# Kernel tuning notes

Measured on AMD Instinct MI355X. Metric: run time of the kernel, lower is better.

The kernel has to match this reference:

```python
import jax, jax.numpy as jnp
import numpy as np

BS, SL, WPL, NP = 32, 256, 4, 320
WD, PD, RD, HD = 768, 64, 64, 256
PN, RN, PL = 32, 64, 8
NF = 128
WINDOW_SIZES = (2, 3, 4)
FD = 2 * HD  # node feature dim


def setup_inputs() -> dict:
    key = jax.random.key(0)
    ks = jax.random.split(key, 24)
    s = 0.02
    inp = {}
    # forward tensors (bert_out stands in for BertModel output after CLS slice)
    inp["bert_out"] = jax.random.normal(ks[0], (BS, NP, WD), jnp.float32)
    inp["wordpiece_gather_idx"] = jax.random.randint(ks[1], (BS, SL, WPL), 0, NP + 1)
    inp["pos"] = jax.random.randint(ks[2], (BS, SL), 0, PN)
    inp["deprel"] = jax.random.randint(ks[3], (BS, SL), 0, RN)
    inp["path"] = jax.random.randint(ks[4], (BS, SL, PL), 0, 2 * SL + 1)
    inp["aspect_head"] = jax.random.randint(ks[5], (BS, SL), 0, SL + 1)
    inp["text_mask"] = jax.random.randint(ks[6], (BS, SL), 0, 2)
    inp["aspect_mask"] = jax.random.randint(ks[7], (BS, SL), 0, 2)
    # parameters (pad row 0 zeroed to mimic padding_idx)
    inp["pos_emb"] = (jax.random.normal(ks[8], (PN, PD)) * s).at[0].set(0.0)
    inp["deprel_emb"] = (jax.random.normal(ks[9], (RN, RD)) * s).at[0].set(0.0)
    inp["pathdepth_emb"] = (jax.random.normal(ks[10], (PL + 2, PD)) * s).at[0].set(0.0)
    inp["ext_rel"] = jax.random.normal(ks[11], (RD,)) * s
    inp["fc1_W"] = jax.random.normal(ks[12], (WD + 2 * PD, FD)) * s
    inp["fc1_b"] = jnp.zeros((FD,), jnp.float32)
    inp["bilin_W"] = jax.random.normal(ks[13], (2 * FD, RD)) * s
    inp["bilin_b"] = jnp.zeros((), jnp.float32)
    inp["W_k2"] = jax.random.normal(ks[14], (2, FD, NF)) * s
    inp["b_k2"] = jnp.zeros((NF,), jnp.float32)
    inp["W_k3"] = jax.random.normal(ks[15], (3, FD, NF)) * s
    inp["b_k3"] = jnp.zeros((NF,), jnp.float32)
    inp["W_k4"] = jax.random.normal(ks[16], (4, FD, NF)) * s
    inp["b_k4"] = jnp.zeros((NF,), jnp.float32)
    inp["fc_out_W"] = jax.random.normal(ks[17], (NF * 3, 3)) * s
    inp["fc_out_b"] = jnp.zeros((3,), jnp.float32)
    return inp


def reference(bert_out, wordpiece_gather_idx, pos, deprel, path, aspect_head,
              text_mask, aspect_mask, pos_emb, deprel_emb, pathdepth_emb, ext_rel,
              fc1_W, fc1_b, bilin_W, bilin_b,
              W_k2, b_k2, W_k3, b_k3, W_k4, b_k4, fc_out_W, fc_out_b):
    bs, sl = pos.shape
    wd = bert_out.shape[-1]
    fd = fc1_b.shape[0]
    # --- wordpiece -> word averaging (pad piece 0 is a zero vector) ---
    pieces = jnp.concatenate([jnp.zeros((bs, 1, wd), bert_out.dtype), bert_out], axis=1)  # [B, NP+1, WD]
    g = jnp.take_along_axis(pieces, wordpiece_gather_idx.reshape(bs, -1)[..., None], axis=1)
    g = g.reshape(bs, sl, -1, wd)                                   # [B, SL, WPL, WD]
    npieces = (wordpiece_gather_idx != 0).sum(-1, keepdims=True)    # [B, SL, 1]
    word = g.sum(2) / jnp.maximum(npieces, 1).astype(g.dtype)       # [B, SL, WD]
    # --- node features ---
    path_depth = (path != 0).sum(-1)                                # [B, SL]
    node_in = jnp.concatenate([word, pos_emb[pos], pathdepth_emb[path_depth]], -1)
    node = jax.nn.relu(node_in @ fc1_W + fc1_b)                     # [B, SL, FD]
    # --- edge features: gather head nodes (0 = pad word -> zeros) ---
    node_pad = jnp.concatenate([jnp.zeros((bs, 1, fd), node.dtype), node], axis=1)
    dep = jnp.take_along_axis(node_pad, aspect_head[..., None], axis=1)  # [B, SL, FD]
    head_text = jnp.concatenate([dep, node], axis=1)                # [B, 2SL, FD]
    tail_text = jnp.concatenate([node, jnp.zeros_like(node)], axis=1)
    edge = jnp.concatenate([head_text, tail_text], axis=-1)         # [B, 2SL, 2FD]
    label = jnp.concatenate([deprel_emb[deprel],
                             jnp.broadcast_to(ext_rel, (bs, sl, ext_rel.shape[0]))], axis=1)
    # bilinear score: x1^T W x2 + b, single output channel
    score = jax.nn.sigmoid(jnp.einsum('bnd,dr,bnr->bn', edge, bilin_W, label) + bilin_b)
    edge_score = jnp.concatenate([jnp.ones((bs, 1), score.dtype), score], axis=1)  # [B, 2SL+1]
    # --- node weight: product of edge scores along dependency path ---
    nw = jnp.prod(jnp.take_along_axis(edge_score[:, None, :], path, axis=2), -1)   # [B, SL]
    nw = jnp.where((text_mask != 0) & (aspect_mask == 0), nw, jnp.zeros_like(nw))
    weight_norm = nw.sum(-1)                                        # [B]
    # --- manual windowed CNN + max pool ---
    pooled = []
    for W, b in ((W_k2, b_k2), (W_k3, b_k3), (W_k4, b_k4)):
        kw = W.shape[0]
        cn = sl - kw + 1
        w_win = jnp.mean(jnp.stack([nw[:, k:k + cn] for k in range(kw)], -1), -1)  # [B, CN]
        y = sum(jnp.einsum('bnf,fm->bnm', node[:, k:k + cn, :], W[k]) for k in range(kw))
        y = w_win[..., None] * y + b                                # [B, CN, NF]
        pooled.append(y.max(axis=1))                                # [B, NF]
    sentence = jnp.concatenate(pooled, -1)
    predicts = sentence @ fc_out_W + fc_out_b                       # [B, 3]
    return predicts, weight_norm
```

## Files before the change

### kernel.cpp

```cpp
#include <hip/hip_runtime.h>
#include <hip/hip_bf16.h>
#include <math.h>

#define BSZ 32
#define SL 256
#define WPL 4
#define NP 320
#define WD 768
#define PD 64
#define RD 64
#define FD 512
#define PL 8
#define NF 128
#define ES_STRIDE 513
#define MROWS (BSZ * SL)
#define NZ 384
#define KZ 2048

typedef __attribute__((ext_vector_type(8))) short bf16x8;
typedef __attribute__((ext_vector_type(4))) float f32x4;
typedef unsigned short ushort_t;
typedef __attribute__((ext_vector_type(4))) ushort_t u16x4;

__device__ __forceinline__ ushort_t f2bf(float x) {
    __hip_bfloat16 h = __float2bfloat16(x);
    return *reinterpret_cast<ushort_t*>(&h);
}
__device__ __forceinline__ float bf2f(ushort_t u) {
    return __uint_as_float(((unsigned)u) << 16);
}

#define NB_GATHER MROWS
#define B_WW   NB_GATHER
#define NB_WW  384
#define B_TAB  (B_WW + NB_WW)
#define NB_TAB 42
#define B_WZT  (B_TAB + NB_TAB)
#define NB_WZT 576
#define B_PAD  (B_WZT + NB_WZT)
#define NB_PAD 2
#define B_UT   (B_PAD + NB_PAD)
#define NB_UT  258
#define NB_TOTAL (B_UT + NB_UT)

__global__ __launch_bounds__(256) void setup_kernel(
    const float* __restrict__ bert, const int* __restrict__ wgi,
    const int* __restrict__ pos, const int* __restrict__ path,
    const float* __restrict__ pos_emb, const float* __restrict__ pd_emb,
    const float* __restrict__ bilin_W, const float* __restrict__ deprel_emb,
    const float* __restrict__ ext_rel, const float* __restrict__ fc1_W,
    const float* __restrict__ fc1_b,
    const float* __restrict__ W2, const float* __restrict__ W3,
    const float* __restrict__ W4,
    ushort_t* __restrict__ word, int* __restrict__ depth,
    ushort_t* __restrict__ Ww, float* __restrict__ posc, float* __restrict__ pdc,
    ushort_t* __restrict__ WzT, ushort_t* __restrict__ node,
    float* __restrict__ Ut, float* __restrict__ v)
{
    const int tid = threadIdx.x;
    const int blk = blockIdx.x;
    if (blk < NB_GATHER) {
        const int bs = blk;
        const int b = bs >> 8;
        const int* gi = wgi + (size_t)bs * WPL;
        const int i0 = gi[0], i1 = gi[1], i2 = gi[2], i3 = gi[3];
        const int npc = (i0 != 0) + (i1 != 0) + (i2 != 0) + (i3 != 0);
        const float inv = 1.0f / (float)(npc > 1 ? npc : 1);
        if (tid < 192) {
            const float4* r0 = (const float4*)(bert + ((size_t)b * NP + (i0 - 1)) * WD);
            const float4* r1 = (const float4*)(bert + ((size_t)b * NP + (i1 - 1)) * WD);
            const float4* r2 = (const float4*)(bert + ((size_t)b * NP + (i2 - 1)) * WD);
            const float4* r3 = (const float4*)(bert + ((size_t)b * NP + (i3 - 1)) * WD);
            float4 s = make_float4(0.f, 0.f, 0.f, 0.f);
            if (i0) { float4 t = r0[tid]; s.x += t.x; s.y += t.y; s.z += t.z; s.w += t.w; }
            if (i1) { float4 t = r1[tid]; s.x += t.x; s.y += t.y; s.z += t.z; s.w += t.w; }
            if (i2) { float4 t = r2[tid]; s.x += t.x; s.y += t.y; s.z += t.z; s.w += t.w; }
            if (i3) { float4 t = r3[tid]; s.x += t.x; s.y += t.y; s.z += t.z; s.w += t.w; }
            u16x4 o;
            o[0] = f2bf(s.x * inv); o[1] = f2bf(s.y * inv);
            o[2] = f2bf(s.z * inv); o[3] = f2bf(s.w * inv);
            *reinterpret_cast<u16x4*>(&word[(size_t)bs * WD + tid * 4]) = o;
        } else if (tid == 192) {
            const int* pp = path + (size_t)bs * PL;
            int pd = 0;
#pragma unroll
            for (int l = 0; l < PL; ++l) pd += (pp[l] != 0);
            depth[bs] = pd;
        }
        return;
    }
    if (blk < B_TAB) {
        __shared__ float s[32][33];
        const int t = blk - B_WW;
        const int kt = t % 24, nt = t / 24;
#pragma unroll
        for (int i = 0; i < 4; ++i) {
            const int idx = i * 256 + tid;
            const int kk = idx >> 5, nn = idx & 31;
            s[kk][nn] = fc1_W[(size_t)(kt * 32 + kk) * FD + nt * 32 + nn];
        }
        __syncthreads();
#pragma unroll
        for (int i = 0; i < 4; ++i) {
            const int idx = i * 256 + tid;
            const int nn = idx >> 5, kk = idx & 31;
            Ww[(size_t)(nt * 32 + nn) * WD + kt * 32 + kk] = f2bf(s[kk][nn]);
        }
        return;
    }
    if (blk < B_WZT) {
        const int r = blk - B_TAB;
#pragma unroll
        for (int h = 0; h < 2; ++h) {
            const int cc = tid + h * 256;
            if (r < 32) {
                float acc = fc1_b[cc];
#pragma unroll
                for (int j = 0; j < PD; ++j)
                    acc += pos_emb[r * PD + j] * fc1_W[(size_t)(WD + j) * FD + cc];
                posc[(size_t)r * FD + cc] = acc;
            } else {
                const int r2 = r - 32;
                float acc = 0.f;
#pragma unroll
                for (int j = 0; j < PD; ++j)
                    acc += pd_emb[r2 * PD + j] * fc1_W[(size_t)(WD + PD + j) * FD + cc];
                pdc[(size_t)r2 * FD + cc] = acc;
            }
        }
        return;
    }
    if (blk < B_PAD) {
        __shared__ float s[32][33];
        const int t2 = blk - B_WZT;
        const int p = t2 / 64, tt = t2 % 64;
        const int dt = tt & 15, ft = tt >> 4;
        int w, k; const float* src;
        if (p < 2)      { w = 0; k = p;     src = W2; }
        else if (p < 5) { w = 1; k = p - 2; src = W3; }
        else            { w = 2; k = p - 5; src = W4; }
#pragma unroll
        for (int i = 0; i < 4; ++i) {
            const int idx = i * 256 + tid;
            const int dd = idx >> 5, ff = idx & 31;
            s[dd][ff] = src[((size_t)k * FD + dt * 32 + dd) * NF + ft * 32 + ff];
        }
        __syncthreads();
#pragma unroll
        for (int i = 0; i < 4; ++i) {
            const int idx = i * 256 + tid;
            const int ff = idx >> 5, dd = idx & 31;
            WzT[(size_t)(w * NF + ft * 32 + ff) * KZ + k * FD + dt * 32 + dd] = f2bf(s[dd][ff]);
        }
        return;
    }
    if (blk < B_UT) {
        const int local = (blk - B_PAD) * 256 + tid;
#pragma unroll
        for (int j = 0; j < 3; ++j) node[(size_t)MROWS * FD + local * 3 + j] = 0;
        return;
    }
    {
        const int idx = (blk - B_UT) * 256 + tid;
        if (idx < 65536) {
            const int r = idx >> 10, d = idx & 1023;
            float s = 0.f;
#pragma unroll
            for (int j = 0; j < RD; ++j) s += bilin_W[d * RD + j] * deprel_emb[r * RD + j];
            Ut[idx] = s;
        } else if (idx < 65536 + FD) {
            const int d = idx - 65536;
            float s = 0.f;
#pragma unroll
            for (int j = 0; j < RD; ++j) s += bilin_W[d * RD + j] * ext_rel[j];
            v[d] = s;
        }
        return;
    }
}

__global__ __launch_bounds__(256) void gemm_node(
    const ushort_t* __restrict__ A,
    const ushort_t* __restrict__ Bt,
    const int* __restrict__ pos, const int* __restrict__ depth,
    const float* __restrict__ posc, const float* __restrict__ pdc,
    ushort_t* __restrict__ C)
{
    __shared__ ushort_t As[128 * 64];
    __shared__ ushort_t Bs[64 * 64];
    __shared__ int spos[128], sdep[128];
    const int tid = threadIdx.x;
    const int wid = tid >> 6, lane = tid & 63;
    const int wr = wid >> 1, wc = wid & 1;
    const int row0 = blockIdx.y * 128, col0 = blockIdx.x * 64;
    const int lr = lane & 15, lk = lane >> 4;
    if (tid < 128) { spos[tid] = pos[row0 + tid]; sdep[tid] = depth[row0 + tid]; }
    f32x4 acc[4][2] = {};
    const ushort_t* gA0 = A + (size_t)row0 * WD;
    const ushort_t* gB0 = Bt + (size_t)col0 * WD;
    for (int k0 = 0; k0 < WD; k0 += 64) {
#pragma unroll
        for (int i = 0; i < 4; ++i) {
            const int c = i * 256 + (wid << 6) + lane;
            const int r = c >> 3, q = (c & 7) ^ (r & 7);
            __builtin_amdgcn_global_load_lds(
                (const __attribute__((address_space(1))) void*)(gA0 + (size_t)r * WD + k0 + q * 8),
                (__attribute__((address_space(3))) void*)((char*)As + i * 4096 + (wid << 10)),
                16, 0, 0);
        }
#pragma unroll
        for (int i = 0; i < 2; ++i) {
            const int c = i * 256 + (wid << 6) + lane;
            const int r = c >> 3, q = (c & 7) ^ (r & 7);
            __builtin_amdgcn_global_load_lds(
                (const __attribute__((address_space(1))) void*)(gB0 + (size_t)r * WD + k0 + q * 8),
                (__attribute__((address_space(3))) void*)((char*)Bs + i * 4096 + (wid << 10)),
                16, 0, 0);
        }
        __syncthreads();
        bf16x8 af[4][2], bfv[2][2];
#pragma unroll
        for (int m = 0; m < 4; ++m) {
            const int fr = wr * 64 + m * 16 + lr;
#pragma unroll
            for (int ks = 0; ks < 2; ++ks)
                af[m][ks] = *reinterpret_cast<const bf16x8*>(
                    &As[fr * 64 + ((((ks << 2) | lk) ^ (fr & 7)) << 3)]);
        }
#pragma unroll
        for (int n = 0; n < 2; ++n) {
            const int fr = wc * 32 + n * 16 + lr;
#pragma unroll
            for (int ks = 0; ks < 2; ++ks)
                bfv[n][ks] = *reinterpret_cast<const bf16x8*>(
                    &Bs[fr * 64 + ((((ks << 2) | lk) ^ (fr & 7)) << 3)]);
        }
#pragma unroll
        for (int ks = 0; ks < 2; ++ks)
#pragma unroll
            for (int m = 0; m < 4; ++m)
#pragma unroll
                for (int n = 0; n < 2; ++n)
                    acc[m][n] = __builtin_amdgcn_mfma_f32_16x16x32_bf16(
                        af[m][ks], bfv[n][ks], acc[m][n], 0, 0, 0);
        __syncthreads();
    }
#pragma unroll
    for (int n = 0; n < 2; ++n) {
        const int col = col0 + wc * 32 + n * 16 + lr;
#pragma unroll
        for (int m = 0; m < 4; ++m) {
            const f32x4 vv = acc[m][n];
#pragma unroll
            for (int j = 0; j < 4; ++j) {
                const int rloc = wr * 64 + m * 16 + lk * 4 + j;
                const float bv = posc[(size_t)spos[rloc] * FD + col]
                               + pdc[(size_t)sdep[rloc] * FD + col];
                C[(size_t)(row0 + rloc) * FD + col] = f2bf(fmaxf(vv[j] + bv, 0.f));
            }
        }
    }
}

__global__ __launch_bounds__(256) void score_kernel(
    const ushort_t* __restrict__ node, const int* __restrict__ aspect_head,
    const int* __restrict__ deprel, const float* __restrict__ Ut,
    const float* __restrict__ v, const float* __restrict__ bilin_b,
    float* __restrict__ edge_score)
{
    const int g = blockIdx.x * 4 + (threadIdx.x >> 6);
    const int lane = threadIdx.x & 63;
    const int b = g >> 9;
    const int n = g & 511;
    const int d0 = lane * 8;
    typedef __attribute__((ext_vector_type(8))) unsigned short u16x8;
    float sum = 0.f;
    if (n < SL) {
        const int dr = deprel[b * SL + n];
        const int h = aspect_head[b * SL + n];
        const float* uc = Ut + (size_t)dr * 1024;
        const u16x8 nv = *reinterpret_cast<const u16x8*>(&node[((size_t)b * SL + n) * FD + d0]);
        if (h != 0) {
            const u16x8 dv = *reinterpret_cast<const u16x8*>(&node[((size_t)b * SL + (h - 1)) * FD + d0]);
#pragma unroll
            for (int i = 0; i < 8; ++i) sum += bf2f(dv[i]) * uc[d0 + i];
        }
#pragma unroll
        for (int i = 0; i < 8; ++i) sum += bf2f(nv[i]) * uc[FD + d0 + i];
    } else {
        const u16x8 nv = *reinterpret_cast<const u16x8*>(&node[((size_t)b * SL + (n - SL)) * FD + d0]);
#pragma unroll
        for (int i = 0; i < 8; ++i) sum += bf2f(nv[i]) * v[d0 + i];
    }
#pragma unroll
    for (int off = 32; off > 0; off >>= 1) sum += __shfl_xor(sum, off, 64);
    if (lane == 0) {
        const float sc = 1.f / (1.f + expf(-(sum + bilin_b[0])));
        edge_score[b * ES_STRIDE + 1 + n] = sc;
        if (n == 0) edge_score[b * ES_STRIDE] = 1.0f;
    }
}

__global__ __launch_bounds__(256) void nw_kernel(
    const float* __restrict__ edge_score, const int* __restrict__ path,
    const int* __restrict__ text_mask, const int* __restrict__ aspect_mask,
    float* __restrict__ nw, float* __restrict__ weight_norm)
{
    const int b = blockIdx.x, s = threadIdx.x;
    const float* es = edge_score + b * ES_STRIDE;
    const int* pp = path + ((size_t)b * SL + s) * PL;
    float p = 1.f;
#pragma unroll
    for (int l = 0; l < PL; ++l) p *= es[pp[l]];
    if (!(text_mask[b * SL + s] != 0 && aspect_mask[b * SL + s] == 0)) p = 0.f;
    nw[b * SL + s] = p;
    __shared__ float red[256];
    red[s] = p;
    __syncthreads();
    for (int off = 128; off > 0; off >>= 1) {
        if (s < off) red[s] += red[s + off];
        __syncthreads();
    }
    if (s == 0) weight_norm[b] = red[0];
}

__global__ __launch_bounds__(256) void gemm_z_pool(
    const ushort_t* __restrict__ node,
    const ushort_t* __restrict__ WzT,
    const float* __restrict__ nw,
    const float* __restrict__ b2, const float* __restrict__ b3,
    const float* __restrict__ b4,
    float* __restrict__ pmaxp)
{
    __shared__ ushort_t As[128 * 64];
    __shared__ ushort_t Bs[64 * 64];
    const int tid = threadIdx.x;
    const int wid = tid >> 6, lane = tid & 63;
    const int wr = wid >> 1, wc = wid & 1;
    const int row0 = blockIdx.y * 128, col0 = blockIdx.x * 64;
    const int lr = lane & 15, lk = lane >> 4;
    f32x4 acc[4][2] = {};
    const ushort_t* gB0 = WzT + (size_t)col0 * KZ;
    const int Keff = ((col0 >> 7) + 2) * 512;
    for (int k0 = 0; k0 < Keff; k0 += 64) {
        const int koff = k0 >> 9;
        const int d0 = k0 & 511;
        const ushort_t* gA0 = node + (size_t)(row0 + koff) * FD + d0;
#pragma unroll
        for (int i = 0; i < 4; ++i) {
            const int c = i * 256 + (wid << 6) + lane;
            const int r = c >> 3, q = (c & 7) ^ (r & 7);
            __builtin_amdgcn_global_load_lds(
                (const __attribute__((address_space(1))) void*)(gA0 + (size_t)r * FD + q * 8),
                (__attribute__((address_space(3))) void*)((char*)As + i * 4096 + (wid << 10)),
                16, 0, 0);
        }
#pragma unroll
        for (int i = 0; i < 2; ++i) {
            const int c = i * 256 + (wid << 6) + lane;
            const int r = c >> 3, q = (c & 7) ^ (r & 7);
            __builtin_amdgcn_global_load_lds(
                (const __attribute__((address_space(1))) void*)(gB0 + (size_t)r * KZ + k0 + q * 8),
                (__attribute__((address_space(3))) void*)((char*)Bs + i * 4096 + (wid << 10)),
                16, 0, 0);
        }
        __syncthreads();
        bf16x8 af[4][2], bfv[2][2];
#pragma unroll
        for (int m = 0; m < 4; ++m) {
            const int fr = wr * 64 + m * 16 + lr;
#pragma unroll
            for (int ks = 0; ks < 2; ++ks)
                af[m][ks] = *reinterpret_cast<const bf16x8*>(
                    &As[fr * 64 + ((((ks << 2) | lk) ^ (fr & 7)) << 3)]);
        }
#pragma unroll
        for (int n = 0; n < 2; ++n) {
            const int fr = wc * 32 + n * 16 + lr;
#pragma unroll
            for (int ks = 0; ks < 2; ++ks)
                bfv[n][ks] = *reinterpret_cast<const bf16x8*>(
                    &Bs[fr * 64 + ((((ks << 2) | lk) ^ (fr & 7)) << 3)]);
        }
#pragma unroll
        for (int ks = 0; ks < 2; ++ks)
#pragma unroll
            for (int m = 0; m < 4; ++m)
#pragma unroll
                for (int n = 0; n < 2; ++n)
                    acc[m][n] = __builtin_amdgcn_mfma_f32_16x16x32_bf16(
                        af[m][ks], bfv[n][ks], acc[m][n], 0, 0, 0);
        __syncthreads();
    }
    const int bI = row0 >> 8;
    const int nn0 = row0 & 255;
    __shared__ float snw[132];
    if (tid < 132) snw[tid] = (nn0 + tid < SL) ? nw[bI * SL + nn0 + tid] : 0.f;
    __syncthreads();
    float cmax[2];
#pragma unroll
    for (int n = 0; n < 2; ++n) {
        const int col = col0 + wc * 32 + n * 16 + lr;
        const int w = col >> 7;
        const int kw = w + 2;
        const float invk = (w == 0) ? 0.5f : (w == 1) ? (1.f / 3.f) : 0.25f;
        const float bf = ((w == 0) ? b2 : (w == 1) ? b3 : b4)[col & 127];
        const int nmax = SL - kw;
        float mx = -INFINITY;
#pragma unroll
        for (int m = 0; m < 4; ++m) {
            const int rbase = wr * 64 + m * 16 + lk * 4;
            const f32x4 vv = acc[m][n];
#pragma unroll
            for (int j = 0; j < 4; ++j) {
                const int rloc = rbase + j;
                if (nn0 + rloc <= nmax) {
                    float ws = 0.f;
                    for (int k = 0; k < kw; ++k) ws += snw[rloc + k];
                    mx = fmaxf(mx, ws * invk * vv[j] + bf);
                }
            }
        }
        mx = fmaxf(mx, __shfl_xor(mx, 16));
        mx = fmaxf(mx, __shfl_xor(mx, 32));
        cmax[n] = mx;
    }
    if (lane < 16) {
#pragma unroll
        for (int n = 0; n < 2; ++n) {
            const int col = col0 + wc * 32 + n * 16 + lr;
            pmaxp[((size_t)blockIdx.y * 2 + wr) * NZ + col] = cmax[n];
        }
    }
}

__global__ __launch_bounds__(384) void finish_kernel(
    const float* __restrict__ pmaxp, const float* __restrict__ W,
    const float* __restrict__ bias, float* __restrict__ out)
{
    const int b = blockIdx.x;
    const int t = threadIdx.x;
    const float* p = pmaxp + (size_t)b * 4 * NZ + t;
    float mx = -INFINITY;
#pragma unroll
    for (int i = 0; i < 4; ++i) mx = fmaxf(mx, p[(size_t)i * NZ]);
    __shared__ float sent[384];
    sent[t] = mx;
    __syncthreads();
    if (t < 3) {
        float acc = bias[t];
        for (int i = 0; i < 384; ++i) acc = fmaf(sent[i], W[i * 3 + t], acc);
        out[b * 3 + t] = acc;
    }
}

extern "C" void kernel_launch(void* const* d_in, const int* in_sizes, int n_in,
                              void* d_out, int out_size, void* d_ws, size_t ws_size,
                              hipStream_t stream)
{
    const float* bert      = (const float*)d_in[0];
    const int*   wgi       = (const int*)d_in[1];
    const int*   pos       = (const int*)d_in[2];
    const int*   deprel    = (const int*)d_in[3];
    const int*   path      = (const int*)d_in[4];
    const int*   ahead     = (const int*)d_in[5];
    const int*   tmask     = (const int*)d_in[6];
    const int*   amask     = (const int*)d_in[7];
    const float* pos_emb   = (const float*)d_in[8];
    const float* dre_emb   = (const float*)d_in[9];
    const float* pd_emb    = (const float*)d_in[10];
    const float* ext_rel   = (const float*)d_in[11];
    const float* fc1_W     = (const float*)d_in[12];
    const float* fc1_b     = (const float*)d_in[13];
    const float* bilin_W   = (const float*)d_in[14];
    const float* bilin_b   = (const float*)d_in[15];
    const float* W2        = (const float*)d_in[16];
    const float* b2        = (const float*)d_in[17];
    const float* W3        = (const float*)d_in[18];
    const float* b3        = (const float*)d_in[19];
    const float* W4        = (const float*)d_in[20];
    const float* b4        = (const float*)d_in[21];
    const float* fco_W     = (const float*)d_in[22];
    const float* fco_b     = (const float*)d_in[23];
    float* out = (float*)d_out;

    uint8_t* w = (uint8_t*)d_ws;
    size_t off = 0;
    ushort_t* word = (ushort_t*)(w + off); off += (size_t)MROWS * WD * 2;
    ushort_t* node = (ushort_t*)(w + off); off += (size_t)(MROWS + 3) * FD * 2;
    ushort_t* Ww   = (ushort_t*)(w + off); off += (size_t)FD * WD * 2;
    ushort_t* WzT  = (ushort_t*)(w + off); off += (size_t)NZ * KZ * 2;
    float* Ut    = (float*)(w + off); off += (size_t)64 * 1024 * 4;
    float* vvec  = (float*)(w + off); off += FD * 4;
    float* posc  = (float*)(w + off); off += (size_t)32 * FD * 4;
    float* pdc   = (float*)(w + off); off += (size_t)10 * FD * 4;
    float* es    = (float*)(w + off); off += (size_t)BSZ * ES_STRIDE * 4;
    float* nw    = (float*)(w + off); off += (size_t)BSZ * SL * 4;
    float* pmaxp = (float*)(w + off); off += (size_t)128 * NZ * 4;
    int*   depth = (int*)(w + off);  off += (size_t)MROWS * 4;

    setup_kernel<<<NB_TOTAL, 256, 0, stream>>>(
        bert, wgi, pos, path, pos_emb, pd_emb,
        bilin_W, dre_emb, ext_rel, fc1_W, fc1_b, W2, W3, W4,
        word, depth, Ww, posc, pdc, WzT, node, Ut, vvec);

    gemm_node<<<dim3(FD / 64, MROWS / 128), 256, 0, stream>>>(
        word, Ww, pos, depth, posc, pdc, node);

    score_kernel<<<(BSZ * 2 * SL) / 4, 256, 0, stream>>>(
        node, ahead, deprel, Ut, vvec, bilin_b, es);

    nw_kernel<<<BSZ, 256, 0, stream>>>(es, path, tmask, amask, nw, out + 96);

    gemm_z_pool<<<dim3(NZ / 64, MROWS / 128), 256, 0, stream>>>(
        node, WzT, nw, b2, b3, b4, pmaxp);

    finish_kernel<<<BSZ, 384, 0, stream>>>(pmaxp, fco_W, fco_b, out);
}
```

Baseline: 112.8 us.

## Load A fragments directly to registers and double-buffer B in both GEMMs

Both MFMA GEMM kernels move from 4 waves of 64x32 tiles to 2 waves of 64x64 tiles (128 threads). The A operand is now loaded straight from global memory into registers instead of being staged through LDS, and the B tile is double-buffered in LDS so the next k-step's loads overlap the current step's MFMAs. This cuts LDS traffic and hides load latency, but it raises register pressure (16 accumulators plus two A fragment sets) and halves the threads per block, which may hurt occupancy and latency hiding.

```diff
diff --git a/kernel.cpp b/kernel.cpp
--- a/kernel.cpp
+++ b/kernel.cpp
@@ -179,81 +179,85 @@
     }
 }
 
-__global__ __launch_bounds__(256) void gemm_node(
+__global__ __launch_bounds__(128) void gemm_node(
     const ushort_t* __restrict__ A,
     const ushort_t* __restrict__ Bt,
     const int* __restrict__ pos, const int* __restrict__ depth,
     const float* __restrict__ posc, const float* __restrict__ pdc,
     ushort_t* __restrict__ C)
 {
-    __shared__ ushort_t As[128 * 64];
-    __shared__ ushort_t Bs[64 * 64];
+    __shared__ ushort_t Bs[2][64 * 64];
     __shared__ int spos[128], sdep[128];
     const int tid = threadIdx.x;
     const int wid = tid >> 6, lane = tid & 63;
-    const int wr = wid >> 1, wc = wid & 1;
     const int row0 = blockIdx.y * 128, col0 = blockIdx.x * 64;
     const int lr = lane & 15, lk = lane >> 4;
-    if (tid < 128) { spos[tid] = pos[row0 + tid]; sdep[tid] = depth[row0 + tid]; }
-    f32x4 acc[4][2] = {};
-    const ushort_t* gA0 = A + (size_t)row0 * WD;
+    spos[tid] = pos[row0 + tid];
+    sdep[tid] = depth[row0 + tid];
+    f32x4 acc[4][4] = {};
+    const ushort_t* gA = A + (size_t)(row0 + wid * 64 + lr) * WD + lk * 8;
     const ushort_t* gB0 = Bt + (size_t)col0 * WD;
-    for (int k0 = 0; k0 < WD; k0 += 64) {
+
+    bf16x8 afA[4][2], afB[4][2];
+    auto loadA = [&](bf16x8 (&af)[4][2], int k0) {
+#pragma unroll
+        for (int m = 0; m < 4; ++m)
+#pragma unroll
+            for (int ks = 0; ks < 2; ++ks)
+                af[m][ks] = *reinterpret_cast<const bf16x8*>(
+                    gA + (size_t)m * 16 * WD + k0 + ks * 32);
+    };
+    auto stageB = [&](ushort_t* buf, int k0) {
 #pragma unroll
         for (int i = 0; i < 4; ++i) {
-            const int c = i * 256 + (wid << 6) + lane;
-            const int r = c >> 3, q = (c & 7) ^ (r & 7);
-            __builtin_amdgcn_global_load_lds(
-                (const __attribute__((address_space(1))) void*)(gA0 + (size_t)r * WD + k0 + q * 8),
-                (__attribute__((address_space(3))) void*)((char*)As + i * 4096 + (wid << 10)),
-                16, 0, 0);
-        }
-#pragma unroll
-        for (int i = 0; i < 2; ++i) {
-            const int c = i * 256 + (wid << 6) + lane;
+            const int c = i * 128 + tid;
             const int r = c >> 3, q = (c & 7) ^ (r & 7);
             __builtin_amdgcn_global_load_lds(
                 (const __attribute__((address_space(1))) void*)(gB0 + (size_t)r * WD + k0 + q * 8),
-                (__attribute__((address_space(3))) void*)((char*)Bs + i * 4096 + (wid << 10)),
+                (__attribute__((address_space(3))) void*)((char*)buf + c * 16),
                 16, 0, 0);
         }
-        __syncthreads();
-        bf16x8 af[4][2], bfv[2][2];
-#pragma unroll
-        for (int m = 0; m < 4; ++m) {
-            const int fr = wr * 64 + m * 16 + lr;
-#pragma unroll
-            for (int ks = 0; ks < 2; ++ks)
-                af[m][ks] = *reinterpret_cast<const bf16x8*>(
-                    &As[fr * 64 + ((((ks << 2) | lk) ^ (fr & 7)) << 3)]);
-        }
-#pragma unroll
-        for (int n = 0; n < 2; ++n) {
-            const int fr = wc * 32 + n * 16 + lr;
+    };
+    auto compute = [&](bf16x8 (&af)[4][2], const ushort_t* buf) {
+        bf16x8 bfv[4][2];
+#pragma unroll
+        for (int n = 0; n < 4; ++n) {
+            const int fr = n * 16 + lr;
 #pragma unroll
             for (int ks = 0; ks < 2; ++ks)
                 bfv[n][ks] = *reinterpret_cast<const bf16x8*>(
-                    &Bs[fr * 64 + ((((ks << 2) | lk) ^ (fr & 7)) << 3)]);
+                    &buf[fr * 64 + ((((ks << 2) | lk) ^ (fr & 7)) << 3)]);
         }
 #pragma unroll
         for (int ks = 0; ks < 2; ++ks)
 #pragma unroll
             for (int m = 0; m < 4; ++m)
 #pragma unroll
-                for (int n = 0; n < 2; ++n)
+                for (int n = 0; n < 4; ++n)
                     acc[m][n] = __builtin_amdgcn_mfma_f32_16x16x32_bf16(
                         af[m][ks], bfv[n][ks], acc[m][n], 0, 0, 0);
-        __syncthreads();
-    }
-#pragma unroll
-    for (int n = 0; n < 2; ++n) {
-        const int col = col0 + wc * 32 + n * 16 + lr;
+    };
+
+    loadA(afA, 0);
+    stageB(Bs[0], 0);
+#pragma unroll 1
+    for (int t = 0; t < 12; t += 2) {
+        __syncthreads();
+        if (t + 1 < 12) { loadA(afB, (t + 1) * 64); stageB(Bs[1], (t + 1) * 64); }
+        compute(afA, Bs[0]);
+        __syncthreads();
+        if (t + 2 < 12) { loadA(afA, (t + 2) * 64); stageB(Bs[0], (t + 2) * 64); }
+        compute(afB, Bs[1]);
+    }
+#pragma unroll
+    for (int n = 0; n < 4; ++n) {
+        const int col = col0 + n * 16 + lr;
 #pragma unroll
         for (int m = 0; m < 4; ++m) {
             const f32x4 vv = acc[m][n];
 #pragma unroll
             for (int j = 0; j < 4; ++j) {
-                const int rloc = wr * 64 + m * 16 + lk * 4 + j;
+                const int rloc = wid * 64 + m * 16 + lk * 4 + j;
                 const float bv = posc[(size_t)spos[rloc] * FD + col]
                                + pdc[(size_t)sdep[rloc] * FD + col];
                 C[(size_t)(row0 + rloc) * FD + col] = f2bf(fmaxf(vv[j] + bv, 0.f));
@@ -324,7 +328,7 @@
     if (s == 0) weight_norm[b] = red[0];
 }
 
-__global__ __launch_bounds__(256) void gemm_z_pool(
+__global__ __launch_bounds__(128) void gemm_z_pool(
     const ushort_t* __restrict__ node,
     const ushort_t* __restrict__ WzT,
     const float* __restrict__ nw,
@@ -332,75 +336,77 @@
     const float* __restrict__ b4,
     float* __restrict__ pmaxp)
 {
-    __shared__ ushort_t As[128 * 64];
-    __shared__ ushort_t Bs[64 * 64];
+    __shared__ ushort_t Bs[2][64 * 64];
+    __shared__ float snw[132];
     const int tid = threadIdx.x;
     const int wid = tid >> 6, lane = tid & 63;
-    const int wr = wid >> 1, wc = wid & 1;
     const int row0 = blockIdx.y * 128, col0 = blockIdx.x * 64;
     const int lr = lane & 15, lk = lane >> 4;
-    f32x4 acc[4][2] = {};
+    f32x4 acc[4][4] = {};
+    const ushort_t* gA = node + (size_t)(row0 + wid * 64 + lr) * FD + lk * 8;
     const ushort_t* gB0 = WzT + (size_t)col0 * KZ;
-    const int Keff = ((col0 >> 7) + 2) * 512;
-    for (int k0 = 0; k0 < Keff; k0 += 64) {
-        const int koff = k0 >> 9;
-        const int d0 = k0 & 511;
-        const ushort_t* gA0 = node + (size_t)(row0 + koff) * FD + d0;
+    const int T = ((col0 >> 7) + 2) * 8;
+
+    bf16x8 afA[4][2], afB[4][2];
+    auto loadA = [&](bf16x8 (&af)[4][2], int k0) {
+#pragma unroll
+        for (int m = 0; m < 4; ++m)
+#pragma unroll
+            for (int ks = 0; ks < 2; ++ks)
+                af[m][ks] = *reinterpret_cast<const bf16x8*>(
+                    gA + (size_t)m * 16 * FD + k0 + ks * 32);
+    };
+    auto stageB = [&](ushort_t* buf, int k0) {
 #pragma unroll
         for (int i = 0; i < 4; ++i) {
-            const int c = i * 256 + (wid << 6) + lane;
-            const int r = c >> 3, q = (c & 7) ^ (r & 7);
-            __builtin_amdgcn_global_load_lds(
-                (const __attribute__((address_space(1))) void*)(gA0 + (size_t)r * FD + q * 8),
-                (__attribute__((address_space(3))) void*)((char*)As + i * 4096 + (wid << 10)),
-                16, 0, 0);
-        }
-#pragma unroll
-        for (int i = 0; i < 2; ++i) {
-            const int c = i * 256 + (wid << 6) + lane;
+            const int c = i * 128 + tid;
             const int r = c >> 3, q = (c & 7) ^ (r & 7);
             __builtin_amdgcn_global_load_lds(
                 (const __attribute__((address_space(1))) void*)(gB0 + (size_t)r * KZ + k0 + q * 8),
-                (__attribute__((address_space(3))) void*)((char*)Bs + i * 4096 + (wid << 10)),
+                (__attribute__((address_space(3))) void*)((char*)buf + c * 16),
                 16, 0, 0);
         }
-        __syncthreads();
-        bf16x8 af[4][2], bfv[2][2];
-#pragma unroll
-        for (int m = 0; m < 4; ++m) {
-            const int fr = wr * 64 + m * 16 + lr;
-#pragma unroll
-            for (int ks = 0; ks < 2; ++ks)
-                af[m][ks] = *reinterpret_cast<const bf16x8*>(
-                    &As[fr * 64 + ((((ks << 2) | lk) ^ (fr & 7)) << 3)]);
-        }
-#pragma unroll
-        for (int n = 0; n < 2; ++n) {
-            const int fr = wc * 32 + n * 16 + lr;
+    };
+    auto compute = [&](bf16x8 (&af)[4][2], const ushort_t* buf) {
+        bf16x8 bfv[4][2];
+#pragma unroll
+        for (int n = 0; n < 4; ++n) {
+            const int fr = n * 16 + lr;
 #pragma unroll
             for (int ks = 0; ks < 2; ++ks)
                 bfv[n][ks] = *reinterpret_cast<const bf16x8*>(
-                    &Bs[fr * 64 + ((((ks << 2) | lk) ^ (fr & 7)) << 3)]);
+                    &buf[fr * 64 + ((((ks << 2) | lk) ^ (fr & 7)) << 3)]);
         }
 #pragma unroll
         for (int ks = 0; ks < 2; ++ks)
 #pragma unroll
             for (int m = 0; m < 4; ++m)
 #pragma unroll
-                for (int n = 0; n < 2; ++n)
+                for (int n = 0; n < 4; ++n)
                     acc[m][n] = __builtin_amdgcn_mfma_f32_16x16x32_bf16(
                         af[m][ks], bfv[n][ks], acc[m][n], 0, 0, 0);
-        __syncthreads();
+    };
+
+    loadA(afA, 0);
+    stageB(Bs[0], 0);
+#pragma unroll 1
+    for (int t = 0; t < T; t += 2) {
+        __syncthreads();
+        if (t + 1 < T) { loadA(afB, (t + 1) * 64); stageB(Bs[1], (t + 1) * 64); }
+        compute(afA, Bs[0]);
+        __syncthreads();
+        if (t + 2 < T) { loadA(afA, (t + 2) * 64); stageB(Bs[0], (t + 2) * 64); }
+        compute(afB, Bs[1]);
     }
     const int bI = row0 >> 8;
     const int nn0 = row0 & 255;
-    __shared__ float snw[132];
-    if (tid < 132) snw[tid] = (nn0 + tid < SL) ? nw[bI * SL + nn0 + tid] : 0.f;
+    for (int i = tid; i < 132; i += 128)
+        snw[i] = (nn0 + i < SL) ? nw[bI * SL + nn0 + i] : 0.f;
     __syncthreads();
-    float cmax[2];
-#pragma unroll
-    for (int n = 0; n < 2; ++n) {
-        const int col = col0 + wc * 32 + n * 16 + lr;
+    float cmax[4];
+#pragma unroll
+    for (int n = 0; n < 4; ++n) {
+        const int col = col0 + n * 16 + lr;
         const int w = col >> 7;
         const int kw = w + 2;
         const float invk = (w == 0) ? 0.5f : (w == 1) ? (1.f / 3.f) : 0.25f;
@@ -409,7 +415,7 @@
         float mx = -INFINITY;
 #pragma unroll
         for (int m = 0; m < 4; ++m) {
-            const int rbase = wr * 64 + m * 16 + lk * 4;
+            const int rbase = wid * 64 + m * 16 + lk * 4;
             const f32x4 vv = acc[m][n];
 #pragma unroll
             for (int j = 0; j < 4; ++j) {
@@ -427,9 +433,9 @@
     }
     if (lane < 16) {
 #pragma unroll
-        for (int n = 0; n < 2; ++n) {
-            const int col = col0 + wc * 32 + n * 16 + lr;
-            pmaxp[((size_t)blockIdx.y * 2 + wr) * NZ + col] = cmax[n];
+        for (int n = 0; n < 4; ++n) {
+            const int col = col0 + n * 16 + lr;
+            pmaxp[((size_t)blockIdx.y * 2 + wid) * NZ + col] = cmax[n];
         }
     }
 }
@@ -504,7 +510,7 @@
         bilin_W, dre_emb, ext_rel, fc1_W, fc1_b, W2, W3, W4,
         word, depth, Ww, posc, pdc, WzT, node, Ut, vvec);
 
-    gemm_node<<<dim3(FD / 64, MROWS / 128), 256, 0, stream>>>(
+    gemm_node<<<dim3(FD / 64, MROWS / 128), 128, 0, stream>>>(
         word, Ww, pos, depth, posc, pdc, node);
 
     score_kernel<<<(BSZ * 2 * SL) / 4, 256, 0, stream>>>(
@@ -512,7 +518,7 @@
 
     nw_kernel<<<BSZ, 256, 0, stream>>>(es, path, tmask, amask, nw, out + 96);
 
-    gemm_z_pool<<<dim3(NZ / 64, MROWS / 128), 256, 0, stream>>>(
+    gemm_z_pool<<<dim3(NZ / 64, MROWS / 128), 128, 0, stream>>>(
         node, WzT, nw, b2, b3, b4, pmaxp);
 
     finish_kernel<<<BSZ, 384, 0, stream>>>(pmaxp, fco_W, fco_b, out);
```

After: 127.7 us. 13.2% more time.

## Shrink gemm_z_pool tiles to 64x64 and remap block order for XCD locality

Applied to the files above, without the earlier changes.

gemm_z_pool moves from 128x64 tiles with 256 threads to 64x64 tiles with 128 threads. This doubles the grid to 768 blocks to improve occupancy and load balance across the variable-K column groups, and it doubles the pooled partial-max buffer, which finish_kernel now reduces over 8 partials instead of 4. Both GEMM kernels switch to a 1D grid with a block-index remap that puts consecutive blocks on the same XCD, so they share row tiles in L2. The cost is less operand reuse per block and more redundant loads of the B tiles.

```diff
diff --git a/kernel.cpp b/kernel.cpp
--- a/kernel.cpp
+++ b/kernel.cpp
@@ -192,7 +192,8 @@
     const int tid = threadIdx.x;
     const int wid = tid >> 6, lane = tid & 63;
     const int wr = wid >> 1, wc = wid & 1;
-    const int row0 = blockIdx.y * 128, col0 = blockIdx.x * 64;
+    const int orig = (blockIdx.x & 63) * 8 + (blockIdx.x >> 6);
+    const int row0 = (orig >> 3) * 128, col0 = (orig & 7) * 64;
     const int lr = lane & 15, lk = lane >> 4;
     if (tid < 128) { spos[tid] = pos[row0 + tid]; sdep[tid] = depth[row0 + tid]; }
     f32x4 acc[4][2] = {};
@@ -324,7 +325,7 @@
     if (s == 0) weight_norm[b] = red[0];
 }
 
-__global__ __launch_bounds__(256) void gemm_z_pool(
+__global__ __launch_bounds__(128) void gemm_z_pool(
     const ushort_t* __restrict__ node,
     const ushort_t* __restrict__ WzT,
     const float* __restrict__ nw,
@@ -332,51 +333,52 @@
     const float* __restrict__ b4,
     float* __restrict__ pmaxp)
 {
-    __shared__ ushort_t As[128 * 64];
+    __shared__ ushort_t As[64 * 64];
     __shared__ ushort_t Bs[64 * 64];
+    __shared__ float snw[68];
     const int tid = threadIdx.x;
     const int wid = tid >> 6, lane = tid & 63;
-    const int wr = wid >> 1, wc = wid & 1;
-    const int row0 = blockIdx.y * 128, col0 = blockIdx.x * 64;
+    const int orig = (blockIdx.x % 96) * 8 + blockIdx.x / 96;
+    const int ct = orig % 6, rt = orig / 6;
+    const int row0 = rt * 64, col0 = ct * 64;
     const int lr = lane & 15, lk = lane >> 4;
-    f32x4 acc[4][2] = {};
+    f32x4 acc[2][4] = {};
+    const ushort_t* gA0 = node + (size_t)row0 * FD;
     const ushort_t* gB0 = WzT + (size_t)col0 * KZ;
-    const int Keff = ((col0 >> 7) + 2) * 512;
+    const int w = col0 >> 7;
+    const int Keff = (w + 2) * 512;
     for (int k0 = 0; k0 < Keff; k0 += 64) {
-        const int koff = k0 >> 9;
-        const int d0 = k0 & 511;
-        const ushort_t* gA0 = node + (size_t)(row0 + koff) * FD + d0;
-#pragma unroll
-        for (int i = 0; i < 4; ++i) {
-            const int c = i * 256 + (wid << 6) + lane;
+#pragma unroll
+        for (int i = 0; i < 4; ++i) {
+            const int c = i * 128 + tid;
             const int r = c >> 3, q = (c & 7) ^ (r & 7);
             __builtin_amdgcn_global_load_lds(
-                (const __attribute__((address_space(1))) void*)(gA0 + (size_t)r * FD + q * 8),
-                (__attribute__((address_space(3))) void*)((char*)As + i * 4096 + (wid << 10)),
+                (const __attribute__((address_space(1))) void*)(gA0 + (size_t)r * FD + k0 + q * 8),
+                (__attribute__((address_space(3))) void*)((char*)As + (size_t)c * 16),
                 16, 0, 0);
         }
 #pragma unroll
-        for (int i = 0; i < 2; ++i) {
-            const int c = i * 256 + (wid << 6) + lane;
+        for (int i = 0; i < 4; ++i) {
+            const int c = i * 128 + tid;
             const int r = c >> 3, q = (c & 7) ^ (r & 7);
             __builtin_amdgcn_global_load_lds(
                 (const __attribute__((address_space(1))) void*)(gB0 + (size_t)r * KZ + k0 + q * 8),
-                (__attribute__((address_space(3))) void*)((char*)Bs + i * 4096 + (wid << 10)),
+                (__attribute__((address_space(3))) void*)((char*)Bs + (size_t)c * 16),
                 16, 0, 0);
         }
         __syncthreads();
-        bf16x8 af[4][2], bfv[2][2];
-#pragma unroll
-        for (int m = 0; m < 4; ++m) {
-            const int fr = wr * 64 + m * 16 + lr;
+        bf16x8 af[2][2], bfv[4][2];
+#pragma unroll
+        for (int m = 0; m < 2; ++m) {
+            const int fr = wid * 32 + m * 16 + lr;
 #pragma unroll
             for (int ks = 0; ks < 2; ++ks)
                 af[m][ks] = *reinterpret_cast<const bf16x8*>(
                     &As[fr * 64 + ((((ks << 2) | lk) ^ (fr & 7)) << 3)]);
         }
 #pragma unroll
-        for (int n = 0; n < 2; ++n) {
-            const int fr = wc * 32 + n * 16 + lr;
+        for (int n = 0; n < 4; ++n) {
+            const int fr = n * 16 + lr;
 #pragma unroll
             for (int ks = 0; ks < 2; ++ks)
                 bfv[n][ks] = *reinterpret_cast<const bf16x8*>(
@@ -385,31 +387,31 @@
 #pragma unroll
         for (int ks = 0; ks < 2; ++ks)
 #pragma unroll
-            for (int m = 0; m < 4; ++m)
-#pragma unroll
-                for (int n = 0; n < 2; ++n)
+            for (int m = 0; m < 2; ++m)
+#pragma unroll
+                for (int n = 0; n < 4; ++n)
                     acc[m][n] = __builtin_amdgcn_mfma_f32_16x16x32_bf16(
                         af[m][ks], bfv[n][ks], acc[m][n], 0, 0, 0);
         __syncthreads();
     }
     const int bI = row0 >> 8;
     const int nn0 = row0 & 255;
-    __shared__ float snw[132];
-    if (tid < 132) snw[tid] = (nn0 + tid < SL) ? nw[bI * SL + nn0 + tid] : 0.f;
+    for (int i = tid; i < 68; i += 128)
+        snw[i] = (nn0 + i < SL) ? nw[bI * SL + nn0 + i] : 0.f;
     __syncthreads();
-    float cmax[2];
-#pragma unroll
-    for (int n = 0; n < 2; ++n) {
-        const int col = col0 + wc * 32 + n * 16 + lr;
-        const int w = col >> 7;
-        const int kw = w + 2;
-        const float invk = (w == 0) ? 0.5f : (w == 1) ? (1.f / 3.f) : 0.25f;
-        const float bf = ((w == 0) ? b2 : (w == 1) ? b3 : b4)[col & 127];
-        const int nmax = SL - kw;
+    const int kw = w + 2;
+    const float invk = (w == 0) ? 0.5f : (w == 1) ? (1.f / 3.f) : 0.25f;
+    const float* bias = (w == 0) ? b2 : (w == 1) ? b3 : b4;
+    const int nmax = SL - kw;
+    float cmax[4];
+#pragma unroll
+    for (int n = 0; n < 4; ++n) {
+        const int col = col0 + n * 16 + lr;
+        const float bf = bias[col & 127];
         float mx = -INFINITY;
 #pragma unroll
-        for (int m = 0; m < 4; ++m) {
-            const int rbase = wr * 64 + m * 16 + lk * 4;
+        for (int m = 0; m < 2; ++m) {
+            const int rbase = wid * 32 + m * 16 + lk * 4;
             const f32x4 vv = acc[m][n];
 #pragma unroll
             for (int j = 0; j < 4; ++j) {
@@ -427,9 +429,9 @@
     }
     if (lane < 16) {
 #pragma unroll
-        for (int n = 0; n < 2; ++n) {
-            const int col = col0 + wc * 32 + n * 16 + lr;
-            pmaxp[((size_t)blockIdx.y * 2 + wr) * NZ + col] = cmax[n];
+        for (int n = 0; n < 4; ++n) {
+            const int col = col0 + n * 16 + lr;
+            pmaxp[((size_t)rt * 2 + wid) * NZ + col] = cmax[n];
         }
     }
 }
@@ -440,10 +442,10 @@
 {
     const int b = blockIdx.x;
     const int t = threadIdx.x;
-    const float* p = pmaxp + (size_t)b * 4 * NZ + t;
+    const float* p = pmaxp + (size_t)b * 8 * NZ + t;
     float mx = -INFINITY;
 #pragma unroll
-    for (int i = 0; i < 4; ++i) mx = fmaxf(mx, p[(size_t)i * NZ]);
+    for (int i = 0; i < 8; ++i) mx = fmaxf(mx, p[(size_t)i * NZ]);
     __shared__ float sent[384];
     sent[t] = mx;
     __syncthreads();
@@ -496,7 +498,7 @@
     float* pdc   = (float*)(w + off); off += (size_t)10 * FD * 4;
     float* es    = (float*)(w + off); off += (size_t)BSZ * ES_STRIDE * 4;
     float* nw    = (float*)(w + off); off += (size_t)BSZ * SL * 4;
-    float* pmaxp = (float*)(w + off); off += (size_t)128 * NZ * 4;
+    float* pmaxp = (float*)(w + off); off += (size_t)256 * NZ * 4;
     int*   depth = (int*)(w + off);  off += (size_t)MROWS * 4;
 
     setup_kernel<<<NB_TOTAL, 256, 0, stream>>>(
@@ -504,7 +506,7 @@
         bilin_W, dre_emb, ext_rel, fc1_W, fc1_b, W2, W3, W4,
         word, depth, Ww, posc, pdc, WzT, node, Ut, vvec);
 
-    gemm_node<<<dim3(FD / 64, MROWS / 128), 256, 0, stream>>>(
+    gemm_node<<<512, 256, 0, stream>>>(
         word, Ww, pos, depth, posc, pdc, node);
 
     score_kernel<<<(BSZ * 2 * SL) / 4, 256, 0, stream>>>(
@@ -512,7 +514,7 @@
 
     nw_kernel<<<BSZ, 256, 0, stream>>>(es, path, tmask, amask, nw, out + 96);
 
-    gemm_z_pool<<<dim3(NZ / 64, MROWS / 128), 256, 0, stream>>>(
+    gemm_z_pool<<<768, 128, 0, stream>>>(
         node, WzT, nw, b2, b3, b4, pmaxp);
 
     finish_kernel<<<BSZ, 384, 0, stream>>>(pmaxp, fco_W, fco_b, out);
```

Measured after the change: 98.40 us. 12.7% less time.
